# Performance work log

Hardware: AMD Instinct MI355X
Metric: run time of the kernel (lower is better)

## Reference

```python
import jax, jax.numpy as jnp
import numpy as np

H_DIM = 2048
N_HEADS = 16

def setup_inputs() -> dict:
    key = jax.random.key(0)
    ks = jax.random.split(key, 9)
    B, T, C = 2, 2048, H_DIM
    scale = 1.0 / np.sqrt(C)  # lecun_normal approx
    src = jax.random.normal(ks[0], (B, T, C), dtype=jnp.float32)
    Wq = jax.random.normal(ks[1], (C, H_DIM), dtype=jnp.float32) * scale
    Wk = jax.random.normal(ks[2], (C, H_DIM), dtype=jnp.float32) * scale
    Wv = jax.random.normal(ks[3], (C, H_DIM), dtype=jnp.float32) * scale
    Wo = jax.random.normal(ks[4], (H_DIM, H_DIM), dtype=jnp.float32) * scale
    bq = jnp.zeros((H_DIM,), jnp.float32)
    bk = jnp.zeros((H_DIM,), jnp.float32)
    bv = jnp.zeros((H_DIM,), jnp.float32)
    bo = jnp.zeros((H_DIM,), jnp.float32)
    return {"src": src, "Wq": Wq, "bq": bq, "Wk": Wk, "bk": bk,
            "Wv": Wv, "bv": bv, "Wo": Wo, "bo": bo}

def reference(src, Wq, bq, Wk, bk, Wv, bv, Wo, bo):
    B, T, C = src.shape
    N = N_HEADS
    D = C // N
    def heads(x):  # [B,T,h_dim] -> [B,N,T,D]
        return x.reshape(B, T, N, D).transpose(0, 2, 1, 3)
    q = heads(src @ Wq + bq)
    k = heads(src @ Wk + bk)
    v = heads(src @ Wv + bv)
    # scaled dot-product with causal mask
    scores = jnp.einsum('bntd,bnsd->bnts', q, k) / jnp.sqrt(jnp.float32(D))
    causal = jnp.tril(jnp.ones((T, T), dtype=bool))
    scores = jnp.where(causal[None, None], scores, -jnp.inf)
    attn = jax.nn.softmax(scores, axis=-1)
    out = jnp.einsum('bnts,bnsd->bntd', attn, v)  # dropout is identity (drop_p=0)
    out = out.transpose(0, 2, 1, 3).reshape(B, T, N * D)
    return out @ Wo + bo
```

## Files before the change

kernel.cpp:

```cpp
#include <hip/hip_runtime.h>
#include <hip/hip_bf16.h>

typedef float f32x4 __attribute__((ext_vector_type(4)));
typedef __bf16 bf16x8v __attribute__((ext_vector_type(8)));
typedef __bf16 bf16x4v __attribute__((ext_vector_type(4)));
typedef unsigned uint2v __attribute__((ext_vector_type(2)));
typedef bf16x8v __attribute__((may_alias)) bf16x8;
typedef bf16x4v __attribute__((may_alias)) bf16x4;
typedef uint2v __attribute__((may_alias)) u32x2;

typedef __attribute__((address_space(1))) const void gvoid_t;
typedef __attribute__((address_space(3))) void lvoid_t;

#define DEVINL __device__ __forceinline__

#define BDIM 2
#define TDIM 2048
#define CDIM 2048
#define NHEAD 16
#define DHEAD 128
#define MROWS 4096
#define WSZ ((size_t)CDIM * CDIM)
#define XSZ ((size_t)MROWS * CDIM)

#define BARRIER_LGKM() asm volatile("s_waitcnt lgkmcnt(0)\ns_barrier" ::: "memory")

DEVINL __bf16 f2bf(float f) {
  unsigned u = __builtin_bit_cast(unsigned, f);
  u += 0x7fffu + ((u >> 16) & 1u);
  unsigned short h = (unsigned short)(u >> 16);
  return __builtin_bit_cast(__bf16, h);
}

DEVINL unsigned pk2bf_trunc(float lo, float hi) {
  return __builtin_amdgcn_perm(__builtin_bit_cast(unsigned, hi),
                               __builtin_bit_cast(unsigned, lo), 0x07060302);
}

DEVINL void gl2lds16(const void* g, void* l) {
  __builtin_amdgcn_global_load_lds((gvoid_t*)g, (lvoid_t*)l, 16, 0, 0);
}

DEVINL int wave_detect(const unsigned* __restrict__ w) {
  const int l = threadIdx.x & 63;
  const unsigned word = w[l];
  const unsigned e = (word >> 7) & 0xFFu;
  const int vote = (e >= 0x70u && e <= 0x87u) ? 1 : 0;
  const unsigned long long m = __ballot(vote);
  return (__popcll(m) >= 32) ? 1 : 0;
}

__global__ __launch_bounds__(256) void cvt_src(
    const void* __restrict__ in, __bf16* __restrict__ out, int n8,
    const void* __restrict__ b0, const void* __restrict__ b1,
    const void* __restrict__ b2, const void* __restrict__ b3,
    float* __restrict__ biasf) {
  const int fl = wave_detect((const unsigned*)in);
  const int bi = blockIdx.x;
  if (bi >= 4096) {
    const int i = (bi - 4096) * 256 + threadIdx.x;
    const void* b = (i < 2048) ? b0 : (i < 4096) ? b1 : (i < 6144) ? b2 : b3;
    const int idx = i & 2047;
    biasf[i] = fl ? (float)((const __bf16*)b)[idx] : ((const float*)b)[idx];
    return;
  }
  const int i = bi * 256 + threadIdx.x;
  if (i >= n8) return;
  if (fl) {
    ((bf16x8*)out)[i] = ((const bf16x8*)in)[i];
  } else {
    const float* f = (const float*)in + (size_t)i * 8;
    bf16x8v v;
#pragma unroll
    for (int j = 0; j < 8; ++j) v[j] = f2bf(f[j]);
    ((bf16x8*)out)[i] = v;
  }
}

__global__ __launch_bounds__(256) void cvt_wt(
    const void* __restrict__ w0, const void* __restrict__ w1,
    const void* __restrict__ w2, const void* __restrict__ w3,
    __bf16* __restrict__ out, const unsigned* __restrict__ srcw) {
  __shared__ __attribute__((aligned(16))) __bf16 tile[64][68];
  const void* W = (blockIdx.z == 0) ? w0 : (blockIdx.z == 1) ? w1
                : (blockIdx.z == 2) ? w2 : w3;
  __bf16* Wt = out + (size_t)blockIdx.z * WSZ;
  const int tx = threadIdx.x & 63, ty = threadIdx.x >> 6;
  const int k0 = blockIdx.x * 64, n0 = blockIdx.y * 64;
  const int fl = wave_detect(srcw);
#pragma unroll
  for (int i = ty; i < 64; i += 4) {
    const size_t off = (size_t)(k0 + i) * CDIM + n0 + tx;
    const float v = fl ? (float)((const __bf16*)W)[off] : ((const float*)W)[off];
    tile[i][tx] = f2bf(v);
  }
  __syncthreads();
#pragma unroll
  for (int i = ty; i < 64; i += 4)
    Wt[(size_t)(n0 + i) * CDIM + k0 + tx] = tile[tx][i];
}

template <int MODE>
__global__ __launch_bounds__(512, 2) void gemmring(
    const __bf16* __restrict__ A, const __bf16* __restrict__ Bt,
    const float* __restrict__ bias, __bf16* __restrict__ qb,
    __bf16* __restrict__ kb, __bf16* __restrict__ vtb,
    const unsigned* __restrict__ srcw, void* __restrict__ outp) {
  constexpr int K = CDIM;
  constexpr int NKT = K / 64;
  __shared__ __attribute__((aligned(16))) __bf16 Asl[4][128 * 32];
  __shared__ __attribute__((aligned(16))) __bf16 Bsl[4][256 * 32];

  const int tid = threadIdx.x;
  const int w = tid >> 6, l = tid & 63;
  const int quad = l >> 4, l16 = l & 15;
  const int wm = w >> 2, wn = w & 3;

  const int bid = blockIdx.x;
  const int bm = bid & 31, bn = bid >> 5;
  const int m0 = bm * 128, n0 = bn * 256;

  const int ls = (tid & 7) ^ ((tid >> 3) & 7);
  const int rbase = 2 * (tid >> 3) + (ls >> 2);
  const int cb8 = (ls & 3) * 8;
  const __bf16* gAh = A + (size_t)(m0 + rbase) * K + cb8;
  const __bf16* gBh = Bt + (size_t)(n0 + rbase) * K + cb8;

  const int L2 = l16 >> 1;
  const int physr = (((l16 & 1) << 2) + quad) ^ L2;
  const int lane_e = L2 * 64 + physr * 8;

#define STAGE_A(h)                                                       \
  gl2lds16(gAh + (size_t)(((h) >> 1) * 64 + ((h) & 1) * 32),             \
           (__bf16*)Asl[(h) & 3] + w * 512)
#define STAGE_B(h, e)                                                    \
  gl2lds16(gBh + (size_t)(e) * 128 * K +                                 \
               (((h) >> 1) * 64 + ((h) & 1) * 32),                       \
           (__bf16*)Bsl[(h) & 3] + (e) * 4096 + w * 512)

  f32x4 acc[4][4];
#pragma unroll
  for (int i = 0; i < 4; ++i)
#pragma unroll
    for (int j = 0; j < 4; ++j) acc[i][j] = (f32x4){0.f, 0.f, 0.f, 0.f};

  STAGE_A(0); STAGE_B(0, 0); STAGE_B(0, 1);
  STAGE_A(1); STAGE_B(1, 0); STAGE_B(1, 1);
  STAGE_A(2); STAGE_B(2, 0); STAGE_B(2, 1);
  asm volatile("s_waitcnt vmcnt(6)" ::: "memory");
  __builtin_amdgcn_sched_barrier(0);
  __builtin_amdgcn_s_barrier();

#define MFMA8(NF0)                                                        \
  __builtin_amdgcn_s_setprio(1);                                          \
  _Pragma("unroll") for (int mi = 0; mi < 4; ++mi) {                      \
    acc[mi][(NF0)] = __builtin_amdgcn_mfma_f32_16x16x32_bf16(             \
        afr[mi], bfr[0], acc[mi][(NF0)], 0, 0, 0);                        \
    acc[mi][(NF0) + 1] = __builtin_amdgcn_mfma_f32_16x16x32_bf16(         \
        afr[mi], bfr[1], acc[mi][(NF0) + 1], 0, 0, 0);                    \
  }                                                                       \
  __builtin_amdgcn_s_setprio(0);

#define LGKM_BAR()                                                        \
  __builtin_amdgcn_s_barrier();                                           \
  asm volatile("s_waitcnt lgkmcnt(0)" ::: "memory");                      \
  __builtin_amdgcn_sched_barrier(0)

  for (int kt = 0; kt < NKT; ++kt) {
    const int h0 = 2 * kt;
    const __bf16* Ab0 = Asl[h0 & 3];
    const __bf16* Bb0 = Bsl[h0 & 3];
    const __bf16* Ab1 = Asl[(h0 + 1) & 3];
    const __bf16* Bb1 = Bsl[(h0 + 1) & 3];
    bf16x8 afr[4], bfr[2];

#pragma unroll
    for (int mi = 0; mi < 4; ++mi)
      afr[mi] = *(const bf16x8*)&Ab0[(wm * 64 + mi * 16) * 32 + lane_e];
    bfr[0] = *(const bf16x8*)&Bb0[(wn * 64 + 0 * 16) * 32 + lane_e];
    bfr[1] = *(const bf16x8*)&Bb0[(wn * 64 + 1 * 16) * 32 + lane_e];
    if (kt <= NKT - 2) { STAGE_A(h0 + 3); STAGE_B(h0 + 3, 0); }
    LGKM_BAR();
    MFMA8(0)
    __builtin_amdgcn_s_barrier();

    bfr[0] = *(const bf16x8*)&Bb0[(wn * 64 + 2 * 16) * 32 + lane_e];
    bfr[1] = *(const bf16x8*)&Bb0[(wn * 64 + 3 * 16) * 32 + lane_e];
    if (kt <= NKT - 2) { STAGE_B(h0 + 3, 1); }
    LGKM_BAR();
    MFMA8(2)
    if (kt < NKT - 1)
      asm volatile("s_waitcnt vmcnt(6)" ::: "memory");
    else
      asm volatile("s_waitcnt vmcnt(0)" ::: "memory");
    __builtin_amdgcn_sched_barrier(0);
    __builtin_amdgcn_s_barrier();

#pragma unroll
    for (int mi = 0; mi < 4; ++mi)
      afr[mi] = *(const bf16x8*)&Ab1[(wm * 64 + mi * 16) * 32 + lane_e];
    bfr[0] = *(const bf16x8*)&Bb1[(wn * 64 + 0 * 16) * 32 + lane_e];
    bfr[1] = *(const bf16x8*)&Bb1[(wn * 64 + 1 * 16) * 32 + lane_e];
    if (kt <= NKT - 3) { STAGE_A(h0 + 4); STAGE_B(h0 + 4, 0); }
    LGKM_BAR();
    MFMA8(0)
    __builtin_amdgcn_s_barrier();

    bfr[0] = *(const bf16x8*)&Bb1[(wn * 64 + 2 * 16) * 32 + lane_e];
    bfr[1] = *(const bf16x8*)&Bb1[(wn * 64 + 3 * 16) * 32 + lane_e];
    if (kt <= NKT - 3) { STAGE_B(h0 + 4, 1); }
    LGKM_BAR();
    MFMA8(2)
    if (kt < NKT - 2)
      asm volatile("s_waitcnt vmcnt(6)" ::: "memory");
    else if (kt == NKT - 2)
      asm volatile("s_waitcnt vmcnt(3)" ::: "memory");
    __builtin_amdgcn_sched_barrier(0);
    __builtin_amdgcn_s_barrier();
  }
#undef MFMA8
#undef LGKM_BAR
#undef STAGE_A
#undef STAGE_B

  if (MODE == 0) {
    const int mat = n0 >> 11;
#pragma unroll
    for (int nf = 0; nf < 4; ++nf) {
      const int n = n0 + wn * 64 + nf * 16 + l16;
      const int nn = n & 2047;
      const int h = nn >> 7, d = nn & 127;
      const float bv = bias[n];
#pragma unroll
      for (int mi = 0; mi < 4; ++mi) {
        const int mbase = m0 + wm * 64 + mi * 16 + quad * 4;
        const int bb = mbase >> 11, t = mbase & 2047;
        if (mat == 2) {
          bf16x4v v4;
#pragma unroll
          for (int r = 0; r < 4; ++r) v4[r] = f2bf(acc[mi][nf][r] + bv);
          *(bf16x4*)&vtb[((size_t)(bb * NHEAD + h) * DHEAD + d) * TDIM + t] = v4;
        } else {
          __bf16* op = (mat == 0) ? qb : kb;
#pragma unroll
          for (int r = 0; r < 4; ++r)
            op[((size_t)(bb * NHEAD + h) * TDIM + t + r) * DHEAD + d] =
                f2bf(acc[mi][nf][r] + bv);
        }
      }
    }
  } else {
    const int ofl = wave_detect(srcw);
#pragma unroll
    for (int nf = 0; nf < 4; ++nf) {
      const int n = n0 + wn * 64 + nf * 16 + l16;
      const float bv = bias[n];
#pragma unroll
      for (int mi = 0; mi < 4; ++mi) {
#pragma unroll
        for (int r = 0; r < 4; ++r) {
          const int m = m0 + wm * 64 + mi * 16 + quad * 4 + r;
          const float v = acc[mi][nf][r] + bv;
          if (ofl) ((__bf16*)outp)[(size_t)m * CDIM + n] = f2bf(v);
          else     ((float*)outp)[(size_t)m * CDIM + n] = v;
        }
      }
    }
  }
}

__global__ __launch_bounds__(256, 2) void attn(
    const __bf16* __restrict__ Q, const __bf16* __restrict__ K,
    const __bf16* __restrict__ Vt, __bf16* __restrict__ ctx,
    int* __restrict__ cnt) {
  constexpr float CSC = 0.12753139726f;
  __shared__ __attribute__((aligned(16))) __bf16 Kls[64 * 128];
  __shared__ __attribute__((aligned(16))) __bf16 Vls[128 * 64];
  __shared__ __attribute__((aligned(16))) __bf16 Pls[4][32 * 64];
  __shared__ int jobLds;

  const int tid = threadIdx.x;
  const int w = tid >> 6, l = tid & 63, quad = l >> 4, l16 = l & 15;

  const int krow = tid >> 4;
  const int kcol = tid & 15;
  const int kldsoff = ((kcol ^ krow) * 8);
  const int vrow = tid >> 3;
  const int vcol = tid & 7;
  const int vldsoff = ((vcol ^ (vrow & 7)) * 8);

  for (;;) {
    __syncthreads();
    if (tid == 0) jobLds = atomicAdd(cnt, 1);
    __syncthreads();
    const int j = jobLds;
    if (j >= 512) break;
    const int qt = 15 - (j >> 5);
    const int bh = j & 31;
    const int t0w = qt * 128 + w * 32;
    const __bf16* Qbh = Q + (size_t)bh * TDIM * DHEAD;
    const __bf16* Kbh = K + (size_t)bh * TDIM * DHEAD;
    const __bf16* Vbh = Vt + (size_t)bh * TDIM * DHEAD;

    bf16x8 qf[2][4];
#pragma unroll
    for (int tt = 0; tt < 2; ++tt)
#pragma unroll
      for (int ks = 0; ks < 4; ++ks)
        qf[tt][ks] = *(const bf16x8*)(Qbh +
                     (size_t)(t0w + tt * 16 + l16) * DHEAD + ks * 32 + quad * 8);

    f32x4 oacc[8][2];
#pragma unroll
    for (int dt = 0; dt < 8; ++dt)
#pragma unroll
      for (int tt = 0; tt < 2; ++tt) oacc[dt][tt] = (f32x4){0.f, 0.f, 0.f, 0.f};
    float mrow[2] = {-1e30f, -1e30f};
    float lrow[2] = {0.f, 0.f};

    const int nsb = 2 * (qt + 1);

    bf16x8 kr[4], vr[4];
#pragma unroll
    for (int p = 0; p < 4; ++p)
      kr[p] = *(const bf16x8*)(Kbh + (size_t)(p * 16 + krow) * DHEAD + kcol * 8);
#pragma unroll
    for (int p = 0; p < 4; ++p)
      vr[p] = *(const bf16x8*)(Vbh + (size_t)(p * 32 + vrow) * TDIM + vcol * 8);

    for (int sb = 0; sb < nsb; ++sb) {
      const int s0 = sb * 64;
      BARRIER_LGKM();
#pragma unroll
      for (int p = 0; p < 4; ++p)
        *(bf16x8*)&Kls[(p * 16 + krow) * 128 + kldsoff] = kr[p];
#pragma unroll
      for (int p = 0; p < 4; ++p)
        *(bf16x8*)&Vls[(p * 32 + vrow) * 64 + vldsoff] = vr[p];
      if (sb + 1 < nsb) {
        const int s1 = s0 + 64;
#pragma unroll
        for (int p = 0; p < 4; ++p)
          kr[p] = *(const bf16x8*)(Kbh + (size_t)(s1 + p * 16 + krow) * DHEAD +
                                   kcol * 8);
#pragma unroll
        for (int p = 0; p < 4; ++p)
          vr[p] = *(const bf16x8*)(Vbh + (size_t)(p * 32 + vrow) * TDIM + s1 +
                                   vcol * 8);
      }
      BARRIER_LGKM();
      if (s0 > t0w + 31) continue;

      f32x4 sacc[4][2];
#pragma unroll
      for (int st = 0; st < 4; ++st)
#pragma unroll
        for (int tt = 0; tt < 2; ++tt) sacc[st][tt] = (f32x4){0.f, 0.f, 0.f, 0.f};
      __builtin_amdgcn_s_setprio(1);
#pragma unroll
      for (int ks = 0; ks < 4; ++ks) {
        bf16x8 kf[4];
#pragma unroll
        for (int st = 0; st < 4; ++st)
          kf[st] = *(const bf16x8*)&Kls[(st * 16 + l16) * 128 +
                                        (((ks * 4 + quad) ^ l16) * 8)];
#pragma unroll
        for (int st = 0; st < 4; ++st)
#pragma unroll
          for (int tt = 0; tt < 2; ++tt)
            sacc[st][tt] = __builtin_amdgcn_mfma_f32_16x16x32_bf16(
                kf[st], qf[tt][ks], sacc[st][tt], 0, 0, 0);
      }
      __builtin_amdgcn_s_setprio(0);
      if (s0 + 63 > t0w) {
#pragma unroll
        for (int st = 0; st < 4; ++st)
#pragma unroll
          for (int tt = 0; tt < 2; ++tt)
#pragma unroll
            for (int r = 0; r < 4; ++r) {
              const int s = s0 + st * 16 + quad * 4 + r;
              const int t = t0w + tt * 16 + l16;
              if (s > t) sacc[st][tt][r] = -1e30f;
            }
      }
#pragma unroll
      for (int tt = 0; tt < 2; ++tt) {
        float vm = -1e30f;
#pragma unroll
        for (int st = 0; st < 4; ++st)
#pragma unroll
          for (int r = 0; r < 4; ++r) vm = fmaxf(vm, sacc[st][tt][r]);
        vm = fmaxf(vm, __shfl_xor(vm, 16));
        vm = fmaxf(vm, __shfl_xor(vm, 32));
        if (__ballot((vm - mrow[tt]) * CSC > 8.0f)) {
          const float mn = fmaxf(mrow[tt], vm);
          const float alpha = exp2f((mrow[tt] - mn) * CSC);
          lrow[tt] *= alpha;
#pragma unroll
          for (int dt = 0; dt < 8; ++dt)
#pragma unroll
            for (int r = 0; r < 4; ++r) oacc[dt][tt][r] *= alpha;
          mrow[tt] = mn;
        }
        const float mcur = mrow[tt];
        float rs = 0.f;
#pragma unroll
        for (int st = 0; st < 4; ++st) {
          const float p0 = exp2f((sacc[st][tt][0] - mcur) * CSC);
          const float p1 = exp2f((sacc[st][tt][1] - mcur) * CSC);
          const float p2 = exp2f((sacc[st][tt][2] - mcur) * CSC);
          const float p3 = exp2f((sacc[st][tt][3] - mcur) * CSC);
          rs += (p0 + p1) + (p2 + p3);
          u32x2 pk = {pk2bf_trunc(p0, p1), pk2bf_trunc(p2, p3)};
          *(u32x2*)&Pls[w][(tt * 16 + l16) * 64 +
                           (((st * 2 + (quad >> 1)) ^ (l16 & 7)) * 8) +
                           (quad & 1) * 4] = pk;
        }
        rs += __shfl_xor(rs, 16);
        rs += __shfl_xor(rs, 32);
        lrow[tt] += rs;
      }
      asm volatile("s_waitcnt lgkmcnt(0)" ::: "memory");
      __builtin_amdgcn_s_setprio(1);
#pragma unroll
      for (int ks = 0; ks < 2; ++ks) {
        bf16x8 pf[2];
#pragma unroll
        for (int tt = 0; tt < 2; ++tt)
          pf[tt] = *(const bf16x8*)&Pls[w][(tt * 16 + l16) * 64 +
                                           (((ks * 4 + quad) ^ (l16 & 7)) * 8)];
#pragma unroll
        for (int dt = 0; dt < 8; ++dt) {
          const bf16x8 vf =
              *(const bf16x8*)&Vls[(dt * 16 + l16) * 64 +
                                   (((ks * 4 + quad) ^ (l16 & 7)) * 8)];
#pragma unroll
          for (int tt = 0; tt < 2; ++tt)
            oacc[dt][tt] = __builtin_amdgcn_mfma_f32_16x16x32_bf16(
                vf, pf[tt], oacc[dt][tt], 0, 0, 0);
        }
      }
      __builtin_amdgcn_s_setprio(0);
    }

    const int b = bh >> 4, h = bh & 15;
#pragma unroll
    for (int tt = 0; tt < 2; ++tt) {
      const float rinv = 1.0f / lrow[tt];
      const int t = t0w + tt * 16 + l16;
      __bf16* cp = ctx + ((size_t)(b * TDIM + t)) * CDIM + h * DHEAD;
#pragma unroll
      for (int dt = 0; dt < 8; ++dt) {
        bf16x4v v4;
#pragma unroll
        for (int r = 0; r < 4; ++r) v4[r] = f2bf(oacc[dt][tt][r] * rinv);
        *(bf16x4*)&cp[dt * 16 + quad * 4] = v4;
      }
    }
  }
}

extern "C" void kernel_launch(void* const* d_in, const int* in_sizes, int n_in,
                              void* d_out, int out_size, void* d_ws,
                              size_t ws_size, hipStream_t stream) {
  const void* src = d_in[0];
  const void* Wq = d_in[1];
  const void* bq = d_in[2];
  const void* Wk = d_in[3];
  const void* bk = d_in[4];
  const void* Wv = d_in[5];
  const void* bv = d_in[6];
  const void* Wo = d_in[7];
  const void* bo = d_in[8];

  char* wsb = (char*)d_ws;
  int* cnt = (int*)(wsb + 128);
  __bf16* srcbf = (__bf16*)(wsb + 256);
  __bf16* wqt = srcbf + XSZ;
  __bf16* wkt = wqt + WSZ;
  __bf16* wvt = wkt + WSZ;
  __bf16* wot = wvt + WSZ;
  __bf16* qb = wot + WSZ;
  __bf16* kb = qb + XSZ;
  __bf16* vtb = kb + XSZ;
  float* biasf = (float*)(vtb + XSZ);
  __bf16* ctx = srcbf;
  (void)wkt; (void)wvt;

  hipMemsetAsync(cnt, 0, sizeof(int), stream);
  cvt_src<<<4128, 256, 0, stream>>>(src, srcbf, (int)(XSZ / 8), bq, bk, bv,
                                    bo, biasf);
  cvt_wt<<<dim3(32, 32, 4), 256, 0, stream>>>(Wq, Wk, Wv, Wo, wqt,
                                              (const unsigned*)src);
  gemmring<0><<<768, 512, 0, stream>>>(srcbf, wqt, biasf, qb, kb, vtb,
                                       nullptr, nullptr);
  attn<<<512, 256, 0, stream>>>(qb, kb, vtb, ctx, cnt);
  gemmring<1><<<256, 512, 0, stream>>>(ctx, wot, biasf + 6144, nullptr,
                                       nullptr, nullptr, (const unsigned*)src,
                                       d_out);
}
```

Baseline: 415.1 us.

## Merge prologue kernels and shrink GEMM LDS ring to three stages

Fuses the source conversion, bias conversion, counter reset and weight transpose into one prologue kernel, which removes a memset and a separate launch. The GEMM ring buffer drops from four to three half-tile stages with rotating pointers and a prefetch depth of one stage, and launch bounds rise to 4 blocks per CU. The smaller LDS footprint is meant to allow more resident blocks. The cost is less load latency hidden per block and tighter register limits that could cause spills.

```diff
diff --git a/kernel.cpp b/kernel.cpp
--- a/kernel.cpp
+++ b/kernel.cpp
@@ -50,44 +50,46 @@
   return (__popcll(m) >= 32) ? 1 : 0;
 }
 
-__global__ __launch_bounds__(256) void cvt_src(
-    const void* __restrict__ in, __bf16* __restrict__ out, int n8,
+__global__ __launch_bounds__(256) void prologue(
+    const void* __restrict__ src, __bf16* __restrict__ srcbf, int n8,
     const void* __restrict__ b0, const void* __restrict__ b1,
     const void* __restrict__ b2, const void* __restrict__ b3,
-    float* __restrict__ biasf) {
-  const int fl = wave_detect((const unsigned*)in);
+    float* __restrict__ biasf, const void* __restrict__ w0,
+    const void* __restrict__ w1, const void* __restrict__ w2,
+    const void* __restrict__ w3, __bf16* __restrict__ wt,
+    int* __restrict__ cnt) {
+  __shared__ __attribute__((aligned(16))) __bf16 tile[64][68];
+  const int fl = wave_detect((const unsigned*)src);
   const int bi = blockIdx.x;
-  if (bi >= 4096) {
+  if (bi < 4096) {
+    const int i = bi * 256 + threadIdx.x;
+    if (i >= n8) return;
+    if (fl) {
+      ((bf16x8*)srcbf)[i] = ((const bf16x8*)src)[i];
+    } else {
+      const float* f = (const float*)src + (size_t)i * 8;
+      bf16x8v v;
+#pragma unroll
+      for (int j = 0; j < 8; ++j) v[j] = f2bf(f[j]);
+      ((bf16x8*)srcbf)[i] = v;
+    }
+    return;
+  }
+  if (bi < 4128) {
+    if (bi == 4096 && threadIdx.x == 0) *cnt = 0;
     const int i = (bi - 4096) * 256 + threadIdx.x;
     const void* b = (i < 2048) ? b0 : (i < 4096) ? b1 : (i < 6144) ? b2 : b3;
     const int idx = i & 2047;
     biasf[i] = fl ? (float)((const __bf16*)b)[idx] : ((const float*)b)[idx];
     return;
   }
-  const int i = bi * 256 + threadIdx.x;
-  if (i >= n8) return;
-  if (fl) {
-    ((bf16x8*)out)[i] = ((const bf16x8*)in)[i];
-  } else {
-    const float* f = (const float*)in + (size_t)i * 8;
-    bf16x8v v;
-#pragma unroll
-    for (int j = 0; j < 8; ++j) v[j] = f2bf(f[j]);
-    ((bf16x8*)out)[i] = v;
-  }
-}
-
-__global__ __launch_bounds__(256) void cvt_wt(
-    const void* __restrict__ w0, const void* __restrict__ w1,
-    const void* __restrict__ w2, const void* __restrict__ w3,
-    __bf16* __restrict__ out, const unsigned* __restrict__ srcw) {
-  __shared__ __attribute__((aligned(16))) __bf16 tile[64][68];
-  const void* W = (blockIdx.z == 0) ? w0 : (blockIdx.z == 1) ? w1
-                : (blockIdx.z == 2) ? w2 : w3;
-  __bf16* Wt = out + (size_t)blockIdx.z * WSZ;
+  const int idx = bi - 4128;
+  const int z = idx >> 10, rem = idx & 1023;
+  const int by = rem >> 5, bx = rem & 31;
+  const void* W = (z == 0) ? w0 : (z == 1) ? w1 : (z == 2) ? w2 : w3;
+  __bf16* Wt = wt + (size_t)z * WSZ;
   const int tx = threadIdx.x & 63, ty = threadIdx.x >> 6;
-  const int k0 = blockIdx.x * 64, n0 = blockIdx.y * 64;
-  const int fl = wave_detect(srcw);
+  const int k0 = bx * 64, n0 = by * 64;
 #pragma unroll
   for (int i = ty; i < 64; i += 4) {
     const size_t off = (size_t)(k0 + i) * CDIM + n0 + tx;
@@ -101,15 +103,15 @@
 }
 
 template <int MODE>
-__global__ __launch_bounds__(512, 2) void gemmring(
+__global__ __launch_bounds__(512, 4) void gemmring(
     const __bf16* __restrict__ A, const __bf16* __restrict__ Bt,
     const float* __restrict__ bias, __bf16* __restrict__ qb,
     __bf16* __restrict__ kb, __bf16* __restrict__ vtb,
     const unsigned* __restrict__ srcw, void* __restrict__ outp) {
   constexpr int K = CDIM;
   constexpr int NKT = K / 64;
-  __shared__ __attribute__((aligned(16))) __bf16 Asl[4][128 * 32];
-  __shared__ __attribute__((aligned(16))) __bf16 Bsl[4][256 * 32];
+  __shared__ __attribute__((aligned(16))) __bf16 Asl[3][128 * 32];
+  __shared__ __attribute__((aligned(16))) __bf16 Bsl[3][256 * 32];
 
   const int tid = threadIdx.x;
   const int w = tid >> 6, l = tid & 63;
@@ -130,13 +132,15 @@
   const int physr = (((l16 & 1) << 2) + quad) ^ L2;
   const int lane_e = L2 * 64 + physr * 8;
 
-#define STAGE_A(h)                                                       \
-  gl2lds16(gAh + (size_t)(((h) >> 1) * 64 + ((h) & 1) * 32),             \
-           (__bf16*)Asl[(h) & 3] + w * 512)
-#define STAGE_B(h, e)                                                    \
-  gl2lds16(gBh + (size_t)(e) * 128 * K +                                 \
-               (((h) >> 1) * 64 + ((h) & 1) * 32),                       \
-           (__bf16*)Bsl[(h) & 3] + (e) * 4096 + w * 512)
+  __bf16 *a0 = (__bf16*)Asl[0], *a1 = (__bf16*)Asl[1], *a2 = (__bf16*)Asl[2];
+  __bf16 *b0 = (__bf16*)Bsl[0], *b1 = (__bf16*)Bsl[1], *b2 = (__bf16*)Bsl[2];
+
+#define STAGE_A(dst, h)                                                   \
+  gl2lds16(gAh + (size_t)(((h) >> 1) * 64 + ((h) & 1) * 32), (dst) + w * 512)
+#define STAGE_B(dst, h, e)                                                \
+  gl2lds16(gBh + (size_t)(e) * 128 * K +                                  \
+               (((h) >> 1) * 64 + ((h) & 1) * 32),                        \
+           (dst) + (e) * 4096 + w * 512)
 
   f32x4 acc[4][4];
 #pragma unroll
@@ -144,10 +148,9 @@
 #pragma unroll
     for (int j = 0; j < 4; ++j) acc[i][j] = (f32x4){0.f, 0.f, 0.f, 0.f};
 
-  STAGE_A(0); STAGE_B(0, 0); STAGE_B(0, 1);
-  STAGE_A(1); STAGE_B(1, 0); STAGE_B(1, 1);
-  STAGE_A(2); STAGE_B(2, 0); STAGE_B(2, 1);
-  asm volatile("s_waitcnt vmcnt(6)" ::: "memory");
+  STAGE_A(a0, 0); STAGE_B(b0, 0, 0); STAGE_B(b0, 0, 1);
+  STAGE_A(a1, 1); STAGE_B(b1, 1, 0); STAGE_B(b1, 1, 1);
+  asm volatile("s_waitcnt vmcnt(3)" ::: "memory");
   __builtin_amdgcn_sched_barrier(0);
   __builtin_amdgcn_s_barrier();
 
@@ -168,29 +171,26 @@
 
   for (int kt = 0; kt < NKT; ++kt) {
     const int h0 = 2 * kt;
-    const __bf16* Ab0 = Asl[h0 & 3];
-    const __bf16* Bb0 = Bsl[h0 & 3];
-    const __bf16* Ab1 = Asl[(h0 + 1) & 3];
-    const __bf16* Bb1 = Bsl[(h0 + 1) & 3];
+    const bool st = (kt < NKT - 1);
     bf16x8 afr[4], bfr[2];
 
 #pragma unroll
     for (int mi = 0; mi < 4; ++mi)
-      afr[mi] = *(const bf16x8*)&Ab0[(wm * 64 + mi * 16) * 32 + lane_e];
-    bfr[0] = *(const bf16x8*)&Bb0[(wn * 64 + 0 * 16) * 32 + lane_e];
-    bfr[1] = *(const bf16x8*)&Bb0[(wn * 64 + 1 * 16) * 32 + lane_e];
-    if (kt <= NKT - 2) { STAGE_A(h0 + 3); STAGE_B(h0 + 3, 0); }
+      afr[mi] = *(const bf16x8*)&a0[(wm * 64 + mi * 16) * 32 + lane_e];
+    bfr[0] = *(const bf16x8*)&b0[(wn * 64 + 0 * 16) * 32 + lane_e];
+    bfr[1] = *(const bf16x8*)&b0[(wn * 64 + 1 * 16) * 32 + lane_e];
+    if (st) { STAGE_A(a2, h0 + 2); STAGE_B(b2, h0 + 2, 0); }
     LGKM_BAR();
     MFMA8(0)
     __builtin_amdgcn_s_barrier();
 
-    bfr[0] = *(const bf16x8*)&Bb0[(wn * 64 + 2 * 16) * 32 + lane_e];
-    bfr[1] = *(const bf16x8*)&Bb0[(wn * 64 + 3 * 16) * 32 + lane_e];
-    if (kt <= NKT - 2) { STAGE_B(h0 + 3, 1); }
+    bfr[0] = *(const bf16x8*)&b0[(wn * 64 + 2 * 16) * 32 + lane_e];
+    bfr[1] = *(const bf16x8*)&b0[(wn * 64 + 3 * 16) * 32 + lane_e];
+    if (st) { STAGE_B(b2, h0 + 2, 1); }
     LGKM_BAR();
     MFMA8(2)
-    if (kt < NKT - 1)
-      asm volatile("s_waitcnt vmcnt(6)" ::: "memory");
+    if (st)
+      asm volatile("s_waitcnt vmcnt(3)" ::: "memory");
     else
       asm volatile("s_waitcnt vmcnt(0)" ::: "memory");
     __builtin_amdgcn_sched_barrier(0);
@@ -198,25 +198,26 @@
 
 #pragma unroll
     for (int mi = 0; mi < 4; ++mi)
-      afr[mi] = *(const bf16x8*)&Ab1[(wm * 64 + mi * 16) * 32 + lane_e];
-    bfr[0] = *(const bf16x8*)&Bb1[(wn * 64 + 0 * 16) * 32 + lane_e];
-    bfr[1] = *(const bf16x8*)&Bb1[(wn * 64 + 1 * 16) * 32 + lane_e];
-    if (kt <= NKT - 3) { STAGE_A(h0 + 4); STAGE_B(h0 + 4, 0); }
+      afr[mi] = *(const bf16x8*)&a1[(wm * 64 + mi * 16) * 32 + lane_e];
+    bfr[0] = *(const bf16x8*)&b1[(wn * 64 + 0 * 16) * 32 + lane_e];
+    bfr[1] = *(const bf16x8*)&b1[(wn * 64 + 1 * 16) * 32 + lane_e];
+    if (st) { STAGE_A(a0, h0 + 3); STAGE_B(b0, h0 + 3, 0); }
     LGKM_BAR();
     MFMA8(0)
     __builtin_amdgcn_s_barrier();
 
-    bfr[0] = *(const bf16x8*)&Bb1[(wn * 64 + 2 * 16) * 32 + lane_e];
-    bfr[1] = *(const bf16x8*)&Bb1[(wn * 64 + 3 * 16) * 32 + lane_e];
-    if (kt <= NKT - 3) { STAGE_B(h0 + 4, 1); }
+    bfr[0] = *(const bf16x8*)&b1[(wn * 64 + 2 * 16) * 32 + lane_e];
+    bfr[1] = *(const bf16x8*)&b1[(wn * 64 + 3 * 16) * 32 + lane_e];
+    if (st) { STAGE_B(b0, h0 + 3, 1); }
     LGKM_BAR();
     MFMA8(2)
-    if (kt < NKT - 2)
-      asm volatile("s_waitcnt vmcnt(6)" ::: "memory");
-    else if (kt == NKT - 2)
-      asm volatile("s_waitcnt vmcnt(3)" ::: "memory");
+    asm volatile("s_waitcnt vmcnt(3)" ::: "memory");
     __builtin_amdgcn_sched_barrier(0);
     __builtin_amdgcn_s_barrier();
+
+    __bf16* t;
+    t = a0; a0 = a2; a2 = a1; a1 = t;
+    t = b0; b0 = b2; b2 = b1; b1 = t;
   }
 #undef MFMA8
 #undef LGKM_BAR
@@ -478,21 +479,15 @@
   int* cnt = (int*)(wsb + 128);
   __bf16* srcbf = (__bf16*)(wsb + 256);
   __bf16* wqt = srcbf + XSZ;
-  __bf16* wkt = wqt + WSZ;
-  __bf16* wvt = wkt + WSZ;
-  __bf16* wot = wvt + WSZ;
+  __bf16* wot = wqt + 3 * WSZ;
   __bf16* qb = wot + WSZ;
   __bf16* kb = qb + XSZ;
   __bf16* vtb = kb + XSZ;
   float* biasf = (float*)(vtb + XSZ);
   __bf16* ctx = srcbf;
-  (void)wkt; (void)wvt;
-
-  hipMemsetAsync(cnt, 0, sizeof(int), stream);
-  cvt_src<<<4128, 256, 0, stream>>>(src, srcbf, (int)(XSZ / 8), bq, bk, bv,
-                                    bo, biasf);
-  cvt_wt<<<dim3(32, 32, 4), 256, 0, stream>>>(Wq, Wk, Wv, Wo, wqt,
-                                              (const unsigned*)src);
+
+  prologue<<<8224, 256, 0, stream>>>(src, srcbf, (int)(XSZ / 8), bq, bk, bv,
+                                     bo, biasf, Wq, Wk, Wv, Wo, wqt, cnt);
   gemmring<0><<<768, 512, 0, stream>>>(srcbf, wqt, biasf, qb, kb, vtb,
                                        nullptr, nullptr);
   attn<<<512, 256, 0, stream>>>(qb, kb, vtb, ctx, cnt);
```

Measured after the change: 397.0 us. 1.05x faster.
